# Performance work log

Measured on AMD Instinct MI355X. Metric: run time of the kernel, lower is better.

Reference implementation:

```python
import jax, jax.numpy as jnp
import numpy as np

B, F, T = 64, 256, 1024  # batch, input features, time steps
H, O = 1024, 512         # hidden units, output projection dim


def setup_inputs() -> dict:
    key = jax.random.key(0)
    k = jax.random.split(key, 4)
    scale_x = 1.0 / np.sqrt(F)
    scale_h = 1.0 / np.sqrt(H)
    return {
        "x": jax.random.normal(k[0], (B, F, T), dtype=jnp.float32),
        "Wx": jax.random.normal(k[1], (F, H), dtype=jnp.float32) * scale_x,
        "Wh": jax.random.normal(k[2], (H, H), dtype=jnp.float32) * scale_h,
        "b": jnp.zeros((H,), dtype=jnp.float32),
        "Wout": jax.random.normal(k[3], (H, O), dtype=jnp.float32) * scale_h,
        "bout": jnp.zeros((O,), dtype=jnp.float32),
    }


def reference(x, Wx, Wh, b, Wout, bout):
    # inputs are (B, F, T); tf.unstack(axis=-1) -> per-step (B, F) slices
    xT = jnp.moveaxis(x, -1, 0)  # (T, B, F)
    s0 = jnp.zeros((x.shape[0], Wh.shape[0]), dtype=x.dtype)

    def step(state, xt):
        # simple RNN cell: tanh(x@Wx + s@Wh + b)
        new_state = jnp.tanh(xt @ Wx + state @ Wh + b)
        return new_state, new_state

    _, states = jax.lax.scan(step, s0, xT)       # (T, B, H)
    states = jnp.moveaxis(states, 0, 1)          # (B, T, H) -- tf.stack(axis=1)
    out = states @ Wout + bout                   # per-timestep Dense projection
    return out
```

## Files before the change

### kernel.cpp

```cpp
#include <hip/hip_runtime.h>
#include <math.h>

#define B_ 64
#define F_ 256
#define T_ 1024
#define H_ 1024
#define O_ 512

typedef short short8 __attribute__((ext_vector_type(8)));
typedef float f32x4 __attribute__((ext_vector_type(4)));

__device__ inline float bf2f(unsigned short u) {
    union { unsigned int i; float f; } v; v.i = ((unsigned int)u) << 16; return v.f;
}
__device__ inline unsigned short f2bf(float f) {
    union { float f; unsigned int i; } v; v.f = f;
    unsigned int i = v.i;
    unsigned int r = (i + 0x7fffu + ((i >> 16) & 1u)) >> 16;
    return (unsigned short)r;
}

__global__ void wt_transpose(const float* __restrict__ src,
                             unsigned short* __restrict__ dst, int K, int N) {
    __shared__ float tile[32][33];
    int n0 = blockIdx.x * 32, k0 = blockIdx.y * 32;
    int tx = threadIdx.x, ty = threadIdx.y;
    for (int i = ty; i < 32; i += 8)
        tile[i][tx] = src[(size_t)(k0 + i) * N + n0 + tx];
    __syncthreads();
    for (int i = ty; i < 32; i += 8)
        dst[(size_t)(n0 + i) * K + k0 + tx] = f2bf(tile[tx][i]);
}

__global__ void xpose_x(const float* __restrict__ x, unsigned short* __restrict__ xT) {
    __shared__ float tile[64][65];
    int id = blockIdx.x;
    int b = id >> 6;
    int ft = (id >> 4) & 3;
    int tt = id & 15;
    int f0 = ft * 64, t0 = tt * 64;
    for (int i = threadIdx.x; i < 64 * 64; i += 256) {
        int fl = i >> 6, tl = i & 63;
        tile[fl][tl] = x[((size_t)(b * F_ + f0 + fl)) * T_ + t0 + tl];
    }
    __syncthreads();
    for (int i = threadIdx.x; i < 64 * 64; i += 256) {
        int tl = i >> 6, fl = i & 63;
        xT[((size_t)(t0 + tl) * B_ + b) * F_ + f0 + fl] = f2bf(tile[fl][tl]);
    }
}

__global__ __launch_bounds__(256) void proj_kernel(
    const unsigned short* __restrict__ xT, const unsigned short* __restrict__ WxT,
    const float* __restrict__ bias, unsigned short* __restrict__ S) {
    int nb = blockIdx.x;
    int mb = blockIdx.y;
    int wave = threadIdx.x >> 6, lane = threadIdx.x & 63;
    int col16 = lane & 15, quad = lane >> 4;
    int m0 = mb * 64 + wave * 16;
    int n0 = nb * 64;

    f32x4 acc[4];
    for (int s = 0; s < 4; ++s)
        for (int r = 0; r < 4; ++r) acc[s][r] = 0.0f;

    #pragma unroll
    for (int kc = 0; kc < F_ / 32; ++kc) {
        int k0 = kc * 32 + quad * 8;
        short8 a = *reinterpret_cast<const short8*>(xT + (size_t)(m0 + col16) * F_ + k0);
        #pragma unroll
        for (int s = 0; s < 4; ++s) {
            short8 bfr = *reinterpret_cast<const short8*>(
                WxT + (size_t)(n0 + s * 16 + col16) * F_ + k0);
            acc[s] = __builtin_amdgcn_mfma_f32_16x16x32_bf16(a, bfr, acc[s], 0, 0, 0);
        }
    }
    #pragma unroll
    for (int s = 0; s < 4; ++s) {
        int col = n0 + s * 16 + col16;
        float bb = bias[col];
        #pragma unroll
        for (int r = 0; r < 4; ++r) {
            int row = m0 + quad * 4 + r;
            S[(size_t)row * H_ + col] = f2bf(acc[s][r] + bb);
        }
    }
}

__global__ __launch_bounds__(64) void rnn_step(
    const unsigned short* __restrict__ Sprev, unsigned short* __restrict__ St,
    const unsigned short* __restrict__ WhT) {
    int bm = blockIdx.x & 3, bn = blockIdx.x >> 2;
    int lane = threadIdx.x;
    int col16 = lane & 15, quad = lane >> 4;
    int m0 = bm * 16, n0 = bn * 16;

    f32x4 acc;
    #pragma unroll
    for (int r = 0; r < 4; ++r)
        acc[r] = bf2f(St[(size_t)(m0 + quad * 4 + r) * H_ + n0 + col16]);

    if (Sprev) {
        #pragma unroll 8
        for (int kc = 0; kc < H_ / 32; ++kc) {
            int k0 = kc * 32 + quad * 8;
            short8 a = *reinterpret_cast<const short8*>(
                Sprev + (size_t)(m0 + col16) * H_ + k0);
            short8 bfr = *reinterpret_cast<const short8*>(
                WhT + (size_t)(n0 + col16) * H_ + k0);
            acc = __builtin_amdgcn_mfma_f32_16x16x32_bf16(a, bfr, acc, 0, 0, 0);
        }
    }
    #pragma unroll
    for (int r = 0; r < 4; ++r)
        St[(size_t)(m0 + quad * 4 + r) * H_ + n0 + col16] = f2bf(tanhf(acc[r]));
}

__global__ __launch_bounds__(256) void out_kernel(
    const unsigned short* __restrict__ S, const unsigned short* __restrict__ WoutT,
    const float* __restrict__ bout, float* __restrict__ out) {
    int nb = blockIdx.x;
    int tt = blockIdx.y;
    int wave = threadIdx.x >> 6, lane = threadIdx.x & 63;
    int col16 = lane & 15, quad = lane >> 4;
    int m0 = tt * 64 + wave * 16;
    int n0 = nb * 64;

    f32x4 acc[4];
    for (int s = 0; s < 4; ++s)
        for (int r = 0; r < 4; ++r) acc[s][r] = 0.0f;

    #pragma unroll 4
    for (int kc = 0; kc < H_ / 32; ++kc) {
        int k0 = kc * 32 + quad * 8;
        short8 a = *reinterpret_cast<const short8*>(S + (size_t)(m0 + col16) * H_ + k0);
        #pragma unroll
        for (int s = 0; s < 4; ++s) {
            short8 bfr = *reinterpret_cast<const short8*>(
                WoutT + (size_t)(n0 + s * 16 + col16) * H_ + k0);
            acc[s] = __builtin_amdgcn_mfma_f32_16x16x32_bf16(a, bfr, acc[s], 0, 0, 0);
        }
    }
    #pragma unroll
    for (int s = 0; s < 4; ++s) {
        int col = n0 + s * 16 + col16;
        float bo = bout[col];
        #pragma unroll
        for (int r = 0; r < 4; ++r) {
            int bidx = wave * 16 + quad * 4 + r;
            out[((size_t)bidx * T_ + tt) * O_ + col] = acc[s][r] + bo;
        }
    }
}

extern "C" void kernel_launch(void* const* d_in, const int* in_sizes, int n_in,
                              void* d_out, int out_size, void* d_ws, size_t ws_size,
                              hipStream_t stream) {
    const float* x    = (const float*)d_in[0];
    const float* Wx   = (const float*)d_in[1];
    const float* Wh   = (const float*)d_in[2];
    const float* bias = (const float*)d_in[3];
    const float* Wout = (const float*)d_in[4];
    const float* bout = (const float*)d_in[5];
    float* out = (float*)d_out;

    unsigned short* WhT   = (unsigned short*)d_ws;
    unsigned short* WxT   = WhT + (size_t)H_ * H_;
    unsigned short* WoutT = WxT + (size_t)H_ * F_;
    unsigned short* S     = WoutT + (size_t)O_ * H_;
    unsigned short* xT    = (unsigned short*)d_out;

    wt_transpose<<<dim3(H_ / 32, H_ / 32), dim3(32, 8), 0, stream>>>(Wh, WhT, H_, H_);
    wt_transpose<<<dim3(H_ / 32, F_ / 32), dim3(32, 8), 0, stream>>>(Wx, WxT, F_, H_);
    wt_transpose<<<dim3(O_ / 32, H_ / 32), dim3(32, 8), 0, stream>>>(Wout, WoutT, H_, O_);
    xpose_x<<<dim3(4096), dim3(256), 0, stream>>>(x, xT);

    proj_kernel<<<dim3(16, 1024), dim3(256), 0, stream>>>(xT, WxT, bias, S);

    for (int t = 0; t < T_; ++t) {
        rnn_step<<<dim3(256), dim3(64), 0, stream>>>(
            t ? S + (size_t)(t - 1) * B_ * H_ : nullptr,
            S + (size_t)t * B_ * H_, WhT);
    }

    out_kernel<<<dim3(8, 1024), dim3(256), 0, stream>>>(S, WoutT, bout, out);
}
```

Baseline: 7.055 ms.

## Replace per-step RNN launches with persistent kernel using group flag barriers

Swaps the 1024 per-timestep kernel launches for a single persistent kernel of 64 blocks. Each block keeps its slice of the transposed Wh in registers, and blocks working on the same batch group synchronise through atomic counters in global memory. The aim is to remove launch overhead and the repeated reloading of Wh at every step. In exchange, correctness depends on all 64 blocks being resident at the same time, and the flags are stored in a spare region of the output buffer.

```diff
diff --git a/kernel.cpp b/kernel.cpp
--- a/kernel.cpp
+++ b/kernel.cpp
@@ -6,6 +6,9 @@
 #define T_ 1024
 #define H_ 1024
 #define O_ 512
+
+#define GROUPS 4
+#define BLOCKS_PER_GROUP 16
 
 typedef short short8 __attribute__((ext_vector_type(8)));
 typedef float f32x4 __attribute__((ext_vector_type(4)));
@@ -87,33 +90,59 @@
     }
 }
 
-__global__ __launch_bounds__(64) void rnn_step(
-    const unsigned short* __restrict__ Sprev, unsigned short* __restrict__ St,
-    const unsigned short* __restrict__ WhT) {
-    int bm = blockIdx.x & 3, bn = blockIdx.x >> 2;
-    int lane = threadIdx.x;
-    int col16 = lane & 15, quad = lane >> 4;
-    int m0 = bm * 16, n0 = bn * 16;
-
-    f32x4 acc;
-    #pragma unroll
-    for (int r = 0; r < 4; ++r)
-        acc[r] = bf2f(St[(size_t)(m0 + quad * 4 + r) * H_ + n0 + col16]);
-
-    if (Sprev) {
-        #pragma unroll 8
-        for (int kc = 0; kc < H_ / 32; ++kc) {
-            int k0 = kc * 32 + quad * 8;
-            short8 a = *reinterpret_cast<const short8*>(
-                Sprev + (size_t)(m0 + col16) * H_ + k0);
-            short8 bfr = *reinterpret_cast<const short8*>(
-                WhT + (size_t)(n0 + col16) * H_ + k0);
-            acc = __builtin_amdgcn_mfma_f32_16x16x32_bf16(a, bfr, acc, 0, 0, 0);
-        }
-    }
-    #pragma unroll
-    for (int r = 0; r < 4; ++r)
-        St[(size_t)(m0 + quad * 4 + r) * H_ + n0 + col16] = f2bf(tanhf(acc[r]));
+__global__ __launch_bounds__(256) void rnn_persistent(
+    unsigned short* __restrict__ S, const unsigned short* __restrict__ WhT,
+    unsigned int* __restrict__ cnt) {
+    const int g  = blockIdx.x & 3;
+    const int nb = blockIdx.x >> 2;
+    const int wave = threadIdx.x >> 6, lane = threadIdx.x & 63;
+    const int col16 = lane & 15, quad = lane >> 4;
+    const int ncol = nb * 64 + wave * 16 + col16;
+    const int arow = g * 16 + col16;
+    const int orow = g * 16 + quad * 4;
+
+    short8 bfr[32];
+    #pragma unroll
+    for (int kc = 0; kc < 32; ++kc)
+        bfr[kc] = *reinterpret_cast<const short8*>(
+            WhT + (size_t)ncol * H_ + kc * 32 + quad * 8);
+
+    unsigned int* flag = cnt + g * 64;
+
+    for (int t = 0; t < T_; ++t) {
+        unsigned short* St = S + (size_t)t * B_ * H_;
+        if (t > 0) {
+            const unsigned int target = (unsigned int)(BLOCKS_PER_GROUP * t);
+            while (__hip_atomic_load(flag, __ATOMIC_RELAXED,
+                                     __HIP_MEMORY_SCOPE_AGENT) < target)
+                __builtin_amdgcn_s_sleep(1);
+            __builtin_amdgcn_fence(__ATOMIC_ACQUIRE, "agent");
+        }
+        f32x4 acc;
+        #pragma unroll
+        for (int r = 0; r < 4; ++r)
+            acc[r] = bf2f(St[(size_t)(orow + r) * H_ + ncol]);
+
+        if (t > 0) {
+            const unsigned short* Sp =
+                S + ((size_t)(t - 1) * B_ + arow) * H_ + quad * 8;
+            #pragma unroll
+            for (int kc = 0; kc < 32; ++kc) {
+                short8 a = *reinterpret_cast<const short8*>(Sp + kc * 32);
+                acc = __builtin_amdgcn_mfma_f32_16x16x32_bf16(a, bfr[kc], acc, 0, 0, 0);
+            }
+        }
+        #pragma unroll
+        for (int r = 0; r < 4; ++r)
+            St[(size_t)(orow + r) * H_ + ncol] = f2bf(tanhf(acc[r]));
+
+        __syncthreads();
+        if (threadIdx.x == 0) {
+            __builtin_amdgcn_fence(__ATOMIC_RELEASE, "agent");
+            __hip_atomic_fetch_add(flag, 1u, __ATOMIC_RELAXED,
+                                   __HIP_MEMORY_SCOPE_AGENT);
+        }
+    }
 }
 
 __global__ __launch_bounds__(256) void out_kernel(
@@ -168,7 +197,9 @@
     unsigned short* WxT   = WhT + (size_t)H_ * H_;
     unsigned short* WoutT = WxT + (size_t)H_ * F_;
     unsigned short* S     = WoutT + (size_t)O_ * H_;
-    unsigned short* xT    = (unsigned short*)d_out;
+
+    unsigned short* xT  = (unsigned short*)d_out;
+    unsigned int* flags = (unsigned int*)((char*)d_out + (size_t)112 * 1024 * 1024);
 
     wt_transpose<<<dim3(H_ / 32, H_ / 32), dim3(32, 8), 0, stream>>>(Wh, WhT, H_, H_);
     wt_transpose<<<dim3(H_ / 32, F_ / 32), dim3(32, 8), 0, stream>>>(Wx, WxT, F_, H_);
@@ -177,11 +208,9 @@
 
     proj_kernel<<<dim3(16, 1024), dim3(256), 0, stream>>>(xT, WxT, bias, S);
 
-    for (int t = 0; t < T_; ++t) {
-        rnn_step<<<dim3(256), dim3(64), 0, stream>>>(
-            t ? S + (size_t)(t - 1) * B_ * H_ : nullptr,
-            S + (size_t)t * B_ * H_, WhT);
-    }
+    hipMemsetAsync(flags, 0, GROUPS * 64 * sizeof(unsigned int), stream);
+    rnn_persistent<<<dim3(GROUPS * BLOCKS_PER_GROUP), dim3(256), 0, stream>>>(
+        S, WhT, flags);
 
     out_kernel<<<dim3(8, 1024), dim3(256), 0, stream>>>(S, WoutT, bout, out);
 }
```

Measured after the change: 9.639 ms. 1.37x slower.
